# Kernel optimization log

Measured on AMD Instinct MI355X. Metric: run time of the kernel, lower is better.

Reference implementation:

```python
import jax, jax.numpy as jnp
import numpy as np

NUM_HEADS = 12

def setup_inputs() -> dict:
    key = jax.random.key(0)
    ks = jax.random.split(key, 7)
    B, N, C = 8, 1024, 768
    hd = C // NUM_HEADS
    s = 0.02
    x = jax.random.normal(ks[0], (B, N, C), jnp.float32)
    w_qkv = jax.random.normal(ks[1], (3 * C, C), jnp.float32) * s
    w_v1 = jax.random.normal(ks[2], (C, C), jnp.float32) * s
    w_v2 = jax.random.normal(ks[3], (C, C), jnp.float32) * s
    w_proj = jax.random.normal(ks[4], (C, C), jnp.float32) * s
    b_proj = jnp.zeros((C,), jnp.float32)
    # init: real part ones, imag part zeros, plus small noise so the gate is non-trivial
    base = jnp.concatenate([jnp.ones((1, 1, 1, hd // 2 + 1, 1), jnp.float32),
                            jnp.zeros((1, 1, 1, hd // 2 + 1, 1), jnp.float32)], axis=4)
    complex_weight = base + jax.random.normal(ks[5], base.shape, jnp.float32) * s
    return {"x": x, "w_qkv": w_qkv, "w_v1": w_v1, "w_v2": w_v2,
            "w_proj": w_proj, "b_proj": b_proj, "complex_weight": complex_weight}


def reference(x, w_qkv, w_v1, w_v2, w_proj, b_proj, complex_weight):
    B, N, C = x.shape
    H = NUM_HEADS
    hd = C // H
    scale = hd ** -0.5

    qkv = (x @ w_qkv.T).reshape(B, N, 3, H, hd).transpose(2, 0, 3, 1, 4)
    q, k, v = qkv[0], qkv[1], qkv[2]  # [B,H,N,hd]

    # standard softmax attention (dropout p=0 -> identity)
    attn = jax.nn.softmax(jnp.einsum('bhid,bhjd->bhij', q, k) * scale, axis=-1)

    # graph-Laplacian branch: full-channel Q K^T, symmetrized, ReLU'd
    attn_hat = jnp.einsum('bhid,bhjd->bij', q, k)  # [B,N,N]
    attn_hat = jax.nn.relu((attn_hat + attn_hat.transpose(0, 2, 1)) * 0.5)

    # degree normalization: d -> 1/sqrt(d) where d != 0
    deg = attn_hat.sum(axis=2)  # [B,N]
    dinv = jnp.where(deg != 0, jax.lax.rsqrt(jnp.where(deg != 0, deg, 1.0)), 0.0)
    norm_ah = attn_hat * dinv[:, None, :] * dinv[:, :, None]

    I = jnp.eye(N, dtype=x.dtype)[None]  # [1,N,N]
    L = I - norm_ah
    L2 = jnp.matmul(L - I, L - I)  # == norm_ah @ norm_ah

    v_flat = v.transpose(0, 2, 1, 3).reshape(B, N, C)
    out = jnp.matmul(L2 - I, v_flat) @ w_v1.T - jnp.matmul(L2, v_flat) @ w_v2.T

    # FFT spectral gate on V along head_dim
    weight = complex_weight[..., 0] + 1j * complex_weight[..., 1]  # [1,1,1,hd//2+1]
    fft_v = jnp.fft.rfft(v, axis=3, norm='ortho') * weight
    ifft_v = jnp.fft.irfft(fft_v, n=hd, axis=3, norm='ortho')

    y = jnp.einsum('bhij,bhjd->bhid', attn, ifft_v).transpose(0, 2, 1, 3).reshape(B, N, C)
    y = y @ w_proj.T + b_proj
    return (y + out, attn)
```

## Files before the change

### kernel.cpp

```cpp
#include <hip/hip_runtime.h>
#include <math.h>

#define Bb 8
#define Nn 1024
#define Cc 768
#define Hh 12
#define HD 64
#define LD 2304

typedef __attribute__((ext_vector_type(4))) float f32x4;
typedef __attribute__((ext_vector_type(8))) short bf16x8;
typedef unsigned short u16;

__device__ __forceinline__ u16 f2bf(float x) {
    unsigned u = __float_as_uint(x);
    return (u16)((u + 0x7FFFu + ((u >> 16) & 1u)) >> 16);
}
__device__ __forceinline__ float bf2f(u16 h) {
    return __uint_as_float(((unsigned)h) << 16);
}
__device__ __forceinline__ void split4(float4 v, ushort4& h, ushort4& l) {
    h.x = f2bf(v.x); l.x = f2bf(v.x - bf2f(h.x));
    h.y = f2bf(v.y); l.y = f2bf(v.y - bf2f(h.y));
    h.z = f2bf(v.z); l.z = f2bf(v.z - bf2f(h.z));
    h.w = f2bf(v.w); l.w = f2bf(v.w - bf2f(h.w));
}

template<int BM, int BN, int WGM, int WGN, int CA, int OUT>
__global__ __launch_bounds__(WGM * WGN * 64)
void gemm_ms(const u16* __restrict__ Ah, const u16* __restrict__ Al,
             const float* __restrict__ Af, int lda, long sA1, long sA2,
             const u16* __restrict__ Bh, const u16* __restrict__ Bl,
             int ldb, long sB1, long sB2,
             float* __restrict__ C, u16* __restrict__ Ch, u16* __restrict__ Cl,
             int ldc, long sC1, long sC2,
             const float* __restrict__ add, const float* __restrict__ bias,
             int K, int zdiv, float alpha, int accum)
{
    constexpr int T  = WGM * WGN * 64;
    constexpr int BK = 32;
    constexpr int LK = 40;
    constexpr int WM = BM / WGM, WN = BN / WGN;
    constexpr int FM = WM / 16, FN = WN / 16;

    __shared__ short Ahs[BM * LK];
    __shared__ short Als[BM * LK];
    __shared__ short Bhs[BN * LK];
    __shared__ short Bls[BN * LK];

    int z = blockIdx.z;
    int b1 = z / zdiv, b2 = z - b1 * zdiv;
    long aoff = (long)b1 * sA1 + (long)b2 * sA2;
    if (CA) { Af += aoff; } else { Ah += aoff; Al += aoff; }
    long boff = (long)b1 * sB1 + (long)b2 * sB2;
    Bh += boff; Bl += boff;
    long coff = (long)b1 * sC1 + (long)b2 * sC2;
    if (OUT != 1) { C += coff; if (add) add += coff; }
    if (OUT >= 1) { Ch += coff; Cl += coff; }

    int m0 = blockIdx.x * BM;
    int n0 = blockIdx.y * BN;
    int tid = threadIdx.x;
    int lane = tid & 63, wid = tid >> 6;
    int wrow = (wid / WGN) * WM;
    int wcol = (wid - (wid / WGN) * WGN) * WN;
    int lr = lane & 15;
    int lk = lane >> 4;

    f32x4 acc[FM][FN] = {};

    for (int k0 = 0; k0 < K; k0 += BK) {
#pragma unroll
        for (int idx = tid; idx < BM * 4; idx += T) {
            int row = idx >> 2, kq = idx & 3;
            if (CA) {
                const float* src = &Af[(long)(m0 + row) * lda + k0 + kq * 8];
                float4 v0 = *(const float4*)src;
                float4 v1 = *(const float4*)(src + 4);
                ushort4 h0, l0, h1, l1; split4(v0, h0, l0); split4(v1, h1, l1);
                *(ushort4*)&Ahs[row * LK + kq * 8]     = h0;
                *(ushort4*)&Ahs[row * LK + kq * 8 + 4] = h1;
                *(ushort4*)&Als[row * LK + kq * 8]     = l0;
                *(ushort4*)&Als[row * LK + kq * 8 + 4] = l1;
            } else {
                long g = (long)(m0 + row) * lda + k0 + kq * 8;
                *(bf16x8*)&Ahs[row * LK + kq * 8] = *(const bf16x8*)&Ah[g];
                *(bf16x8*)&Als[row * LK + kq * 8] = *(const bf16x8*)&Al[g];
            }
        }
#pragma unroll
        for (int idx = tid; idx < BN * 4; idx += T) {
            int row = idx >> 2, kq = idx & 3;
            long g = (long)(n0 + row) * ldb + k0 + kq * 8;
            *(bf16x8*)&Bhs[row * LK + kq * 8] = *(const bf16x8*)&Bh[g];
            *(bf16x8*)&Bls[row * LK + kq * 8] = *(const bf16x8*)&Bl[g];
        }
        __syncthreads();

        bf16x8 ah[FM], al[FM];
#pragma unroll
        for (int fm = 0; fm < FM; ++fm) {
            int off = (wrow + fm * 16 + lr) * LK + lk * 8;
            ah[fm] = *(const bf16x8*)&Ahs[off];
            al[fm] = *(const bf16x8*)&Als[off];
        }
#pragma unroll
        for (int fn = 0; fn < FN; ++fn) {
            int off = (wcol + fn * 16 + lr) * LK + lk * 8;
            bf16x8 bh = *(const bf16x8*)&Bhs[off];
            bf16x8 bl = *(const bf16x8*)&Bls[off];
#pragma unroll
            for (int fm = 0; fm < FM; ++fm) {
                acc[fm][fn] = __builtin_amdgcn_mfma_f32_16x16x32_bf16(ah[fm], bh, acc[fm][fn], 0, 0, 0);
                acc[fm][fn] = __builtin_amdgcn_mfma_f32_16x16x32_bf16(al[fm], bh, acc[fm][fn], 0, 0, 0);
                acc[fm][fn] = __builtin_amdgcn_mfma_f32_16x16x32_bf16(ah[fm], bl, acc[fm][fn], 0, 0, 0);
            }
        }
        __syncthreads();
    }

#pragma unroll
    for (int fm = 0; fm < FM; ++fm) {
#pragma unroll
        for (int fn = 0; fn < FN; ++fn) {
            int col = n0 + wcol + fn * 16 + lr;
            float bv = 0.0f;
            if (OUT != 1) { if (bias) bv = bias[col]; }
#pragma unroll
            for (int r = 0; r < 4; ++r) {
                int row = m0 + wrow + fm * 16 + lk * 4 + r;
                long idx = (long)row * ldc + col;
                float v = alpha * acc[fm][fn][r];
                if (OUT != 1) {
                    if (accum) v += C[idx];
                    v += bv;
                    if (add) v += add[idx];
                    C[idx] = v;
                }
                if (OUT >= 1) {
                    u16 hh = f2bf(v);
                    Ch[idx] = hh;
                    Cl[idx] = f2bf(v - bf2f(hh));
                }
            }
        }
    }
}

__device__ inline float waveReduceSum(float v) {
#pragma unroll
    for (int off = 32; off; off >>= 1) v += __shfl_down(v, off, 64);
    return v;
}
__device__ inline float waveReduceMax(float v) {
#pragma unroll
    for (int off = 32; off; off >>= 1) v = fmaxf(v, __shfl_down(v, off, 64));
    return v;
}

__global__ __launch_bounds__(256)
void softmax_rows(float* __restrict__ p)
{
    long row = blockIdx.x;
    float* r = p + row * 1024;
    int tid = threadIdx.x;
    float4 x = ((float4*)r)[tid];
    float m = fmaxf(fmaxf(x.x, x.y), fmaxf(x.z, x.w));
    m = waveReduceMax(m);
    __shared__ float sm[4];
    __shared__ float bm, bs;
    int lane = tid & 63, wid = tid >> 6;
    if (!lane) sm[wid] = m;
    __syncthreads();
    if (tid == 0) bm = fmaxf(fmaxf(sm[0], sm[1]), fmaxf(sm[2], sm[3]));
    __syncthreads();
    float mm = bm;
    x.x = expf(x.x - mm); x.y = expf(x.y - mm);
    x.z = expf(x.z - mm); x.w = expf(x.w - mm);
    float s = x.x + x.y + x.z + x.w;
    s = waveReduceSum(s);
    if (!lane) sm[wid] = s;
    __syncthreads();
    if (tid == 0) bs = sm[0] + sm[1] + sm[2] + sm[3];
    __syncthreads();
    float inv = 1.0f / bs;
    x.x *= inv; x.y *= inv; x.z *= inv; x.w *= inv;
    ((float4*)r)[tid] = x;
}

__global__ __launch_bounds__(256)
void sym_relu(float* __restrict__ AH)
{
    long idx = (long)blockIdx.x * 256 + threadIdx.x;
    if (idx >= (long)Bb * Nn * Nn) return;
    int b = (int)(idx >> 20);
    int r = (int)(idx & 1048575);
    int i = r >> 10, j = r & 1023;
    if (j < i) return;
    float* Ab = AH + ((long)b << 20);
    float t = 0.5f * (Ab[i * 1024 + j] + Ab[j * 1024 + i]);
    t = fmaxf(t, 0.0f);
    Ab[i * 1024 + j] = t;
    Ab[j * 1024 + i] = t;
}

__global__ __launch_bounds__(256)
void deg_dinv(const float* __restrict__ AH, float* __restrict__ dinv)
{
    long row = blockIdx.x;
    const float* r = AH + row * 1024;
    int tid = threadIdx.x;
    float4 x = ((const float4*)r)[tid];
    float s = x.x + x.y + x.z + x.w;
    s = waveReduceSum(s);
    __shared__ float sm[4];
    int lane = tid & 63, wid = tid >> 6;
    if (!lane) sm[wid] = s;
    __syncthreads();
    if (tid == 0) {
        float d = sm[0] + sm[1] + sm[2] + sm[3];
        dinv[row] = (d != 0.0f) ? rsqrtf(d) : 0.0f;
    }
}

__global__ __launch_bounds__(256)
void scale_split(const float* __restrict__ AH, const float* __restrict__ dinv,
                 u16* __restrict__ oh, u16* __restrict__ ol)
{
    long i4 = (long)blockIdx.x * 256 + threadIdx.x;
    if (i4 >= (long)Bb * Nn * Nn / 4) return;
    long e = i4 * 4;
    int b = (int)(e >> 20);
    int i = (int)((e >> 10) & 1023);
    int j = (int)(e & 1023);
    float di = dinv[(b << 10) + i];
    const float* dj = &dinv[(b << 10) + j];
    float4 v = ((const float4*)AH)[i4];
    v.x *= di * dj[0]; v.y *= di * dj[1]; v.z *= di * dj[2]; v.w *= di * dj[3];
    ushort4 h, l; split4(v, h, l);
    ((ushort4*)oh)[i4] = h;
    ((ushort4*)ol)[i4] = l;
}

__global__ __launch_bounds__(256)
void split_plain(const float* __restrict__ in, u16* __restrict__ h,
                 u16* __restrict__ l, long n4)
{
    for (long i = (long)blockIdx.x * 256 + threadIdx.x; i < n4;
         i += (long)gridDim.x * 256) {
        float4 v = ((const float4*)in)[i];
        ushort4 hh, ll; split4(v, hh, ll);
        ((ushort4*)h)[i] = hh;
        ((ushort4*)l)[i] = ll;
    }
}

__global__ __launch_bounds__(256)
void wdiff_split(const float* __restrict__ a, const float* __restrict__ b,
                 u16* __restrict__ h, u16* __restrict__ l, long n4)
{
    for (long i = (long)blockIdx.x * 256 + threadIdx.x; i < n4;
         i += (long)gridDim.x * 256) {
        float4 va = ((const float4*)a)[i];
        float4 vb = ((const float4*)b)[i];
        float4 v = make_float4(va.x - vb.x, va.y - vb.y, va.z - vb.z, va.w - vb.w);
        ushort4 hh, ll; split4(v, hh, ll);
        ((ushort4*)h)[i] = hh;
        ((ushort4*)l)[i] = ll;
    }
}

__global__ __launch_bounds__(256)
void tsplit(const float* __restrict__ in, long sIn, int ldi,
            u16* __restrict__ oh, u16* __restrict__ ol, long sOut, int R)
{
    __shared__ float Ts[64][65];
    int z = blockIdx.z;
    in += (long)z * sIn;
    oh += (long)z * sOut;
    ol += (long)z * sOut;
    int r0 = blockIdx.x * 64;
    int c0 = blockIdx.y * 64;
    int tid = threadIdx.x;
#pragma unroll
    for (int idx = tid; idx < 1024; idx += 256) {
        int r = idx >> 4, c4 = idx & 15;
        float4 v = *(const float4*)&in[(long)(r0 + r) * ldi + c0 + c4 * 4];
        Ts[c4 * 4 + 0][r] = v.x;
        Ts[c4 * 4 + 1][r] = v.y;
        Ts[c4 * 4 + 2][r] = v.z;
        Ts[c4 * 4 + 3][r] = v.w;
    }
    __syncthreads();
#pragma unroll
    for (int idx = tid; idx < 1024; idx += 256) {
        int c = idx >> 4, r4 = idx & 15;
        float4 v = make_float4(Ts[c][r4 * 4], Ts[c][r4 * 4 + 1],
                               Ts[c][r4 * 4 + 2], Ts[c][r4 * 4 + 3]);
        ushort4 h, l; split4(v, h, l);
        long o = (long)(c0 + c) * R + r0 + r4 * 4;
        *(ushort4*)&oh[o] = h;
        *(ushort4*)&ol[o] = l;
    }
}

__global__ void build_g(const float* __restrict__ cw, float* __restrict__ g)
{
    int d = threadIdx.x;
    if (d >= 64) return;
    float s = cw[0] + ((d & 1) ? -cw[64] : cw[64]);
#pragma unroll
    for (int f = 1; f < 32; ++f) {
        int ph = (f * d) & 63;
        float ang = 6.283185307179586f * (float)ph / 64.0f;
        s += 2.0f * (cw[2 * f] * cosf(ang) + cw[2 * f + 1] * sinf(ang));
    }
    g[d] = s * 0.015625f;
}

__global__ __launch_bounds__(256)
void ifv_kernel(const float* __restrict__ qkv, const float* __restrict__ g,
                float* __restrict__ ifv)
{
    int bn = blockIdx.x;
    __shared__ float Vr[768];
    __shared__ float Gs[64];
    const float* vrow = qkv + (long)bn * LD + 2 * Cc;
    int tid = threadIdx.x;
    if (tid < 64) Gs[tid] = g[tid];
    for (int c = tid; c < 768; c += 256) Vr[c] = vrow[c];
    __syncthreads();
    for (int c = tid; c < 768; c += 256) {
        int h = c >> 6, t = c & 63;
        const float* vh = Vr + (h << 6);
        float s = 0.0f;
#pragma unroll
        for (int m2 = 0; m2 < 64; ++m2)
            s = fmaf(vh[m2], Gs[(m2 - t) & 63], s);
        ifv[(long)bn * 768 + c] = s;
    }
}

extern "C" void kernel_launch(void* const* d_in, const int* in_sizes, int n_in,
                              void* d_out, int out_size, void* d_ws, size_t ws_size,
                              hipStream_t stream)
{
    (void)in_sizes; (void)n_in; (void)out_size; (void)ws_size;

    const float* x      = (const float*)d_in[0];
    const float* w_qkv  = (const float*)d_in[1];
    const float* w_v1   = (const float*)d_in[2];
    const float* w_v2   = (const float*)d_in[3];
    const float* w_proj = (const float*)d_in[4];
    const float* b_proj = (const float*)d_in[5];
    const float* cw     = (const float*)d_in[6];

    float* out  = (float*)d_out;
    float* attn = out + (long)Bb * Nn * Cc;

    char* W = (char*)d_ws;
    long off = 0;
    auto alloc = [&](long bytes) { char* p = W + off; off += (bytes + 255) & ~255L; return p; };

    float* QKVf  = (float*)alloc((long)8192 * 2304 * 4);
    u16*   QKVh  = (u16*)  alloc((long)8192 * 2304 * 2);
    u16*   QKVl  = (u16*)  alloc((long)8192 * 2304 * 2);
    u16*   AHh   = (u16*)  alloc((long)Bb * Nn * Nn * 2);
    u16*   AHl   = (u16*)  alloc((long)Bb * Nn * Nn * 2);
    u16*   L2h   = (u16*)  alloc((long)Bb * Nn * Nn * 2);
    u16*   L2l   = (u16*)  alloc((long)Bb * Nn * Nn * 2);
    u16*   MVh   = (u16*)  alloc((long)8192 * 768 * 2);
    u16*   MVl   = (u16*)  alloc((long)8192 * 768 * 2);
    float* IFVf  = (float*)alloc((long)8192 * 768 * 4);
    u16*   IFVTh = (u16*)  alloc((long)Bb * 768 * 1024 * 2);
    u16*   IFVTl = (u16*)  alloc((long)Bb * 768 * 1024 * 2);
    u16*   VTh   = (u16*)  alloc((long)Bb * 768 * 1024 * 2);
    u16*   VTl   = (u16*)  alloc((long)Bb * 768 * 1024 * 2);
    u16*   Yh    = (u16*)  alloc((long)8192 * 768 * 2);
    u16*   Yl    = (u16*)  alloc((long)8192 * 768 * 2);
    float* OUTB  = (float*)alloc((long)8192 * 768 * 4);
    u16*   xh    = (u16*)  alloc((long)8192 * 768 * 2);
    u16*   xl    = (u16*)  alloc((long)8192 * 768 * 2);
    u16*   wqh   = (u16*)  alloc((long)2304 * 768 * 2);
    u16*   wql   = (u16*)  alloc((long)2304 * 768 * 2);
    u16*   wv1h  = (u16*)  alloc((long)768 * 768 * 2);
    u16*   wv1l  = (u16*)  alloc((long)768 * 768 * 2);
    u16*   wdh   = (u16*)  alloc((long)768 * 768 * 2);
    u16*   wdl   = (u16*)  alloc((long)768 * 768 * 2);
    u16*   wph   = (u16*)  alloc((long)768 * 768 * 2);
    u16*   wpl   = (u16*)  alloc((long)768 * 768 * 2);
    float* DINV  = (float*)alloc(8192 * 4);
    float* G     = (float*)alloc(256);

    float* AH = attn;

    const long sQKV = (long)Nn * LD;
    const long sNN  = (long)Nn * Nn;
    const long sNC  = (long)Nn * Cc;

    build_g<<<1, 64, 0, stream>>>(cw, G);
    split_plain<<<2048, 256, 0, stream>>>(x,      xh,   xl,   (long)8192 * 768 / 4);
    split_plain<<<1024, 256, 0, stream>>>(w_qkv,  wqh,  wql,  (long)2304 * 768 / 4);
    split_plain<<<512,  256, 0, stream>>>(w_v1,   wv1h, wv1l, (long)768 * 768 / 4);
    split_plain<<<512,  256, 0, stream>>>(w_proj, wph,  wpl,  (long)768 * 768 / 4);
    wdiff_split<<<512,  256, 0, stream>>>(w_v1, w_v2, wdh, wdl, (long)768 * 768 / 4);

    gemm_ms<128, 128, 2, 2, 0, 2><<<dim3(64, 18, 1), 256, 0, stream>>>(
        xh, xl, nullptr, Cc, 0, 0, wqh, wql, Cc, 0, 0,
        QKVf, QKVh, QKVl, LD, 0, 0, nullptr, nullptr, Cc, 1, 1.0f, 0);

    gemm_ms<128, 128, 2, 2, 0, 0><<<dim3(8, 8, Bb), 256, 0, stream>>>(
        QKVh, QKVl, nullptr, LD, sQKV, 0, QKVh + Cc, QKVl + Cc, LD, sQKV, 0,
        AH, nullptr, nullptr, Nn, sNN, 0, nullptr, nullptr, Cc, 1, 1.0f, 0);

    sym_relu<<<32768, 256, 0, stream>>>(AH);
    deg_dinv<<<Bb * Nn, 256, 0, stream>>>(AH, DINV);
    scale_split<<<8192, 256, 0, stream>>>(AH, DINV, AHh, AHl);

    gemm_ms<128, 128, 2, 2, 0, 1><<<dim3(8, 8, Bb), 256, 0, stream>>>(
        AHh, AHl, nullptr, Nn, sNN, 0, AHh, AHl, Nn, sNN, 0,
        nullptr, L2h, L2l, Nn, sNN, 0, nullptr, nullptr, Nn, 1, 1.0f, 0);

    tsplit<<<dim3(16, 12, Bb), 256, 0, stream>>>(
        QKVf + 2 * Cc, sQKV, LD, VTh, VTl, (long)Cc * Nn, Nn);
    gemm_ms<128, 128, 2, 2, 0, 1><<<dim3(8, 6, Bb), 256, 0, stream>>>(
        L2h, L2l, nullptr, Nn, sNN, 0, VTh, VTl, Nn, (long)Cc * Nn, 0,
        nullptr, MVh, MVl, Cc, sNC, 0, nullptr, nullptr, Nn, 1, 1.0f, 0);

    ifv_kernel<<<Bb * Nn, 256, 0, stream>>>(QKVf, G, IFVf);
    tsplit<<<dim3(16, 12, Bb), 256, 0, stream>>>(
        IFVf, sNC, Cc, IFVTh, IFVTl, (long)Cc * Nn, Nn);

    gemm_ms<128, 128, 2, 2, 0, 0><<<dim3(64, 6, 1), 256, 0, stream>>>(
        QKVh + 2 * Cc, QKVl + 2 * Cc, nullptr, LD, 0, 0, wv1h, wv1l, Cc, 0, 0,
        OUTB, nullptr, nullptr, Cc, 0, 0, nullptr, nullptr, Cc, 1, -1.0f, 0);
    gemm_ms<128, 128, 2, 2, 0, 0><<<dim3(64, 6, 1), 256, 0, stream>>>(
        MVh, MVl, nullptr, Cc, 0, 0, wdh, wdl, Cc, 0, 0,
        OUTB, nullptr, nullptr, Cc, 0, 0, nullptr, nullptr, Cc, 1, 1.0f, 1);

    gemm_ms<128, 128, 2, 2, 0, 0><<<dim3(8, 8, Bb * Hh), 256, 0, stream>>>(
        QKVh, QKVl, nullptr, LD, sQKV, HD, QKVh + Cc, QKVl + Cc, LD, sQKV, HD,
        attn, nullptr, nullptr, Nn, (long)Hh * sNN, sNN,
        nullptr, nullptr, HD, Hh, 0.125f, 0);

    softmax_rows<<<Bb * Hh * Nn, 256, 0, stream>>>(attn);

    gemm_ms<128, 64, 2, 1, 1, 1><<<dim3(8, 1, Bb * Hh), 128, 0, stream>>>(
        nullptr, nullptr, attn, Nn, (long)Hh * sNN, sNN,
        IFVTh, IFVTl, Nn, (long)Cc * Nn, (long)HD * Nn,
        nullptr, Yh, Yl, Cc, sNC, HD, nullptr, nullptr, Nn, Hh, 1.0f, 0);

    gemm_ms<128, 128, 2, 2, 0, 0><<<dim3(64, 6, 1), 256, 0, stream>>>(
        Yh, Yl, nullptr, Cc, 0, 0, wph, wpl, Cc, 0, 0,
        out, nullptr, nullptr, Cc, 0, 0, OUTB, b_proj, Cc, 1, 1.0f, 0);
}
```

Before: 1.561 ms.

## Reassociate L2·V as A(A·V), GEMM-ize FFT gate, register-prefetch GEMM tiles

Instead of forming the N×N matrix norm_ah² and multiplying it by V, the code computes (V^T·A)^T and then A·(A·V), which removes one N³ GEMM per batch in favour of two N²·C GEMMs. The spectral FFT gate becomes a block-circulant 768×768 matrix applied as a GEMM, and transposition now works on the bf16 hi/lo pairs, so the fp32 QKV buffer and the separate ifv kernel are no longer needed. The GEMM kernel gains a BK template parameter and register-staged global prefetch of the next K tile, with one barrier pair per iteration. Several launches also move to 64×64 tiles with BK=64, which raises block count at the cost of less reuse per tile.

```diff
diff --git a/kernel.cpp b/kernel.cpp
--- a/kernel.cpp
+++ b/kernel.cpp
@@ -26,7 +26,7 @@
     h.w = f2bf(v.w); l.w = f2bf(v.w - bf2f(h.w));
 }
 
-template<int BM, int BN, int WGM, int WGN, int CA, int OUT>
+template<int BM, int BN, int BK, int WGM, int WGN, int CA, int OUT>
 __global__ __launch_bounds__(WGM * WGN * 64)
 void gemm_ms(const u16* __restrict__ Ah, const u16* __restrict__ Al,
              const float* __restrict__ Af, int lda, long sA1, long sA2,
@@ -38,15 +38,15 @@
              int K, int zdiv, float alpha, int accum)
 {
     constexpr int T  = WGM * WGN * 64;
-    constexpr int BK = 32;
-    constexpr int LK = 40;
+    constexpr int LK = BK + 8;
     constexpr int WM = BM / WGM, WN = BN / WGN;
     constexpr int FM = WM / 16, FN = WN / 16;
-
-    __shared__ short Ahs[BM * LK];
-    __shared__ short Als[BM * LK];
-    __shared__ short Bhs[BN * LK];
-    __shared__ short Bls[BN * LK];
+    constexpr int KQ = BK / 8;
+    constexpr int AI = BM * BK / 8 / T;
+    constexpr int BI = BN * BK / 8 / T;
+    constexpr int KS = BK / 32;
+
+    __shared__ short Ahs[BM * LK], Als[BM * LK], Bhs[BN * LK], Bls[BN * LK];
 
     int z = blockIdx.z;
     int b1 = z / zdiv, b2 = z - b1 * zdiv;
@@ -55,8 +55,8 @@
     long boff = (long)b1 * sB1 + (long)b2 * sB2;
     Bh += boff; Bl += boff;
     long coff = (long)b1 * sC1 + (long)b2 * sC2;
-    if (OUT != 1) { C += coff; if (add) add += coff; }
-    if (OUT >= 1) { Ch += coff; Cl += coff; }
+    if (OUT == 0) { C += coff; if (add) add += coff; }
+    else          { Ch += coff; Cl += coff; }
 
     int m0 = blockIdx.x * BM;
     int n0 = blockIdx.y * BN;
@@ -69,54 +69,89 @@
 
     f32x4 acc[FM][FN] = {};
 
-    for (int k0 = 0; k0 < K; k0 += BK) {
-#pragma unroll
-        for (int idx = tid; idx < BM * 4; idx += T) {
-            int row = idx >> 2, kq = idx & 3;
+    bf16x8 rah[AI], ral[AI], rbh[BI], rbl[BI];
+    float4 rfa[AI][2];
+
+    auto LOAD = [&](int k0) {
+#pragma unroll
+        for (int i = 0; i < AI; ++i) {
+            int idx = i * T + tid;
+            int row = idx / KQ, kq = idx - row * KQ;
             if (CA) {
-                const float* src = &Af[(long)(m0 + row) * lda + k0 + kq * 8];
-                float4 v0 = *(const float4*)src;
-                float4 v1 = *(const float4*)(src + 4);
-                ushort4 h0, l0, h1, l1; split4(v0, h0, l0); split4(v1, h1, l1);
+                const float* s = &Af[(long)(m0 + row) * lda + k0 + kq * 8];
+                rfa[i][0] = *(const float4*)s;
+                rfa[i][1] = *(const float4*)(s + 4);
+            } else {
+                long g = (long)(m0 + row) * lda + k0 + kq * 8;
+                rah[i] = *(const bf16x8*)&Ah[g];
+                ral[i] = *(const bf16x8*)&Al[g];
+            }
+        }
+#pragma unroll
+        for (int i = 0; i < BI; ++i) {
+            int idx = i * T + tid;
+            int row = idx / KQ, kq = idx - row * KQ;
+            long g = (long)(n0 + row) * ldb + k0 + kq * 8;
+            rbh[i] = *(const bf16x8*)&Bh[g];
+            rbl[i] = *(const bf16x8*)&Bl[g];
+        }
+    };
+    auto STORE = [&]() {
+#pragma unroll
+        for (int i = 0; i < AI; ++i) {
+            int idx = i * T + tid;
+            int row = idx / KQ, kq = idx - row * KQ;
+            if (CA) {
+                ushort4 h0, l0, h1, l1;
+                split4(rfa[i][0], h0, l0); split4(rfa[i][1], h1, l1);
                 *(ushort4*)&Ahs[row * LK + kq * 8]     = h0;
                 *(ushort4*)&Ahs[row * LK + kq * 8 + 4] = h1;
                 *(ushort4*)&Als[row * LK + kq * 8]     = l0;
                 *(ushort4*)&Als[row * LK + kq * 8 + 4] = l1;
             } else {
-                long g = (long)(m0 + row) * lda + k0 + kq * 8;
-                *(bf16x8*)&Ahs[row * LK + kq * 8] = *(const bf16x8*)&Ah[g];
-                *(bf16x8*)&Als[row * LK + kq * 8] = *(const bf16x8*)&Al[g];
+                *(bf16x8*)&Ahs[row * LK + kq * 8] = rah[i];
+                *(bf16x8*)&Als[row * LK + kq * 8] = ral[i];
             }
         }
 #pragma unroll
-        for (int idx = tid; idx < BN * 4; idx += T) {
-            int row = idx >> 2, kq = idx & 3;
-            long g = (long)(n0 + row) * ldb + k0 + kq * 8;
-            *(bf16x8*)&Bhs[row * LK + kq * 8] = *(const bf16x8*)&Bh[g];
-            *(bf16x8*)&Bls[row * LK + kq * 8] = *(const bf16x8*)&Bl[g];
-        }
+        for (int i = 0; i < BI; ++i) {
+            int idx = i * T + tid;
+            int row = idx / KQ, kq = idx - row * KQ;
+            *(bf16x8*)&Bhs[row * LK + kq * 8] = rbh[i];
+            *(bf16x8*)&Bls[row * LK + kq * 8] = rbl[i];
+        }
+    };
+
+    int nt = K / BK;
+    LOAD(0);
+    for (int t = 0; t < nt; ++t) {
         __syncthreads();
-
-        bf16x8 ah[FM], al[FM];
-#pragma unroll
-        for (int fm = 0; fm < FM; ++fm) {
-            int off = (wrow + fm * 16 + lr) * LK + lk * 8;
-            ah[fm] = *(const bf16x8*)&Ahs[off];
-            al[fm] = *(const bf16x8*)&Als[off];
-        }
-#pragma unroll
-        for (int fn = 0; fn < FN; ++fn) {
-            int off = (wcol + fn * 16 + lr) * LK + lk * 8;
-            bf16x8 bh = *(const bf16x8*)&Bhs[off];
-            bf16x8 bl = *(const bf16x8*)&Bls[off];
+        STORE();
+        __syncthreads();
+        if (t + 1 < nt) LOAD((t + 1) * BK);
+
+#pragma unroll
+        for (int s = 0; s < KS; ++s) {
+            bf16x8 fah[FM], fal[FM];
 #pragma unroll
             for (int fm = 0; fm < FM; ++fm) {
-                acc[fm][fn] = __builtin_amdgcn_mfma_f32_16x16x32_bf16(ah[fm], bh, acc[fm][fn], 0, 0, 0);
-                acc[fm][fn] = __builtin_amdgcn_mfma_f32_16x16x32_bf16(al[fm], bh, acc[fm][fn], 0, 0, 0);
-                acc[fm][fn] = __builtin_amdgcn_mfma_f32_16x16x32_bf16(ah[fm], bl, acc[fm][fn], 0, 0, 0);
+                int off = (wrow + fm * 16 + lr) * LK + s * 32 + lk * 8;
+                fah[fm] = *(const bf16x8*)&Ahs[off];
+                fal[fm] = *(const bf16x8*)&Als[off];
             }
-        }
-        __syncthreads();
+#pragma unroll
+            for (int fn = 0; fn < FN; ++fn) {
+                int off = (wcol + fn * 16 + lr) * LK + s * 32 + lk * 8;
+                bf16x8 fbh = *(const bf16x8*)&Bhs[off];
+                bf16x8 fbl = *(const bf16x8*)&Bls[off];
+#pragma unroll
+                for (int fm = 0; fm < FM; ++fm) {
+                    acc[fm][fn] = __builtin_amdgcn_mfma_f32_16x16x32_bf16(fah[fm], fbh, acc[fm][fn], 0, 0, 0);
+                    acc[fm][fn] = __builtin_amdgcn_mfma_f32_16x16x32_bf16(fal[fm], fbh, acc[fm][fn], 0, 0, 0);
+                    acc[fm][fn] = __builtin_amdgcn_mfma_f32_16x16x32_bf16(fah[fm], fbl, acc[fm][fn], 0, 0, 0);
+                }
+            }
+        }
     }
 
 #pragma unroll
@@ -125,19 +160,18 @@
         for (int fn = 0; fn < FN; ++fn) {
             int col = n0 + wcol + fn * 16 + lr;
             float bv = 0.0f;
-            if (OUT != 1) { if (bias) bv = bias[col]; }
+            if (OUT == 0) { if (bias) bv = bias[col]; }
 #pragma unroll
             for (int r = 0; r < 4; ++r) {
                 int row = m0 + wrow + fm * 16 + lk * 4 + r;
                 long idx = (long)row * ldc + col;
                 float v = alpha * acc[fm][fn][r];
-                if (OUT != 1) {
+                if (OUT == 0) {
                     if (accum) v += C[idx];
                     v += bv;
                     if (add) v += add[idx];
                     C[idx] = v;
-                }
-                if (OUT >= 1) {
+                } else {
                     u16 hh = f2bf(v);
                     Ch[idx] = hh;
                     Cl[idx] = f2bf(v - bf2f(hh));
@@ -271,36 +305,38 @@
 }
 
 __global__ __launch_bounds__(256)
-void tsplit(const float* __restrict__ in, long sIn, int ldi,
-            u16* __restrict__ oh, u16* __restrict__ ol, long sOut, int R)
-{
-    __shared__ float Ts[64][65];
+void t16(const u16* __restrict__ inh, const u16* __restrict__ inl, long sIn, int ldi,
+         u16* __restrict__ oh, u16* __restrict__ ol, long sOut, int R)
+{
+    __shared__ u16 Th[64][68];
+    __shared__ u16 Tl[64][68];
     int z = blockIdx.z;
-    in += (long)z * sIn;
-    oh += (long)z * sOut;
-    ol += (long)z * sOut;
+    inh += (long)z * sIn; inl += (long)z * sIn;
+    oh  += (long)z * sOut; ol += (long)z * sOut;
     int r0 = blockIdx.x * 64;
     int c0 = blockIdx.y * 64;
     int tid = threadIdx.x;
 #pragma unroll
-    for (int idx = tid; idx < 1024; idx += 256) {
-        int r = idx >> 4, c4 = idx & 15;
-        float4 v = *(const float4*)&in[(long)(r0 + r) * ldi + c0 + c4 * 4];
-        Ts[c4 * 4 + 0][r] = v.x;
-        Ts[c4 * 4 + 1][r] = v.y;
-        Ts[c4 * 4 + 2][r] = v.z;
-        Ts[c4 * 4 + 3][r] = v.w;
-    }
-    __syncthreads();
-#pragma unroll
-    for (int idx = tid; idx < 1024; idx += 256) {
-        int c = idx >> 4, r4 = idx & 15;
-        float4 v = make_float4(Ts[c][r4 * 4], Ts[c][r4 * 4 + 1],
-                               Ts[c][r4 * 4 + 2], Ts[c][r4 * 4 + 3]);
-        ushort4 h, l; split4(v, h, l);
-        long o = (long)(c0 + c) * R + r0 + r4 * 4;
-        *(ushort4*)&oh[o] = h;
-        *(ushort4*)&ol[o] = l;
+    for (int i = tid; i < 1024; i += 256) {
+        int r = i >> 4, cq = i & 15;
+        ushort4 vh = *(const ushort4*)&inh[(long)(r0 + r) * ldi + c0 + cq * 4];
+        ushort4 vl = *(const ushort4*)&inl[(long)(r0 + r) * ldi + c0 + cq * 4];
+        Th[cq * 4 + 0][r] = vh.x; Th[cq * 4 + 1][r] = vh.y;
+        Th[cq * 4 + 2][r] = vh.z; Th[cq * 4 + 3][r] = vh.w;
+        Tl[cq * 4 + 0][r] = vl.x; Tl[cq * 4 + 1][r] = vl.y;
+        Tl[cq * 4 + 2][r] = vl.z; Tl[cq * 4 + 3][r] = vl.w;
+    }
+    __syncthreads();
+#pragma unroll
+    for (int i = tid; i < 1024; i += 256) {
+        int c = i >> 4, rq = i & 15;
+        ushort4 vh = make_ushort4(Th[c][rq * 4], Th[c][rq * 4 + 1],
+                                  Th[c][rq * 4 + 2], Th[c][rq * 4 + 3]);
+        ushort4 vl = make_ushort4(Tl[c][rq * 4], Tl[c][rq * 4 + 1],
+                                  Tl[c][rq * 4 + 2], Tl[c][rq * 4 + 3]);
+        long o = (long)(c0 + c) * R + r0 + rq * 4;
+        *(ushort4*)&oh[o] = vh;
+        *(ushort4*)&ol[o] = vl;
     }
 }
 
@@ -319,26 +355,16 @@
 }
 
 __global__ __launch_bounds__(256)
-void ifv_kernel(const float* __restrict__ qkv, const float* __restrict__ g,
-                float* __restrict__ ifv)
-{
-    int bn = blockIdx.x;
-    __shared__ float Vr[768];
-    __shared__ float Gs[64];
-    const float* vrow = qkv + (long)bn * LD + 2 * Cc;
-    int tid = threadIdx.x;
-    if (tid < 64) Gs[tid] = g[tid];
-    for (int c = tid; c < 768; c += 256) Vr[c] = vrow[c];
-    __syncthreads();
-    for (int c = tid; c < 768; c += 256) {
-        int h = c >> 6, t = c & 63;
-        const float* vh = Vr + (h << 6);
-        float s = 0.0f;
-#pragma unroll
-        for (int m2 = 0; m2 < 64; ++m2)
-            s = fmaf(vh[m2], Gs[(m2 - t) & 63], s);
-        ifv[(long)bn * 768 + c] = s;
-    }
+void build_gb(const float* __restrict__ g, u16* __restrict__ gbh, u16* __restrict__ gbl)
+{
+    int idx = blockIdx.x * 256 + threadIdx.x;
+    if (idx >= Cc * Cc) return;
+    int c = idx / Cc, c2 = idx - (idx / Cc) * Cc;
+    int h = c >> 6, t = c & 63, h2 = c2 >> 6, m = c2 & 63;
+    float v = (h == h2) ? g[(m - t) & 63] : 0.0f;
+    u16 hh = f2bf(v);
+    gbh[idx] = hh;
+    gbl[idx] = f2bf(v - bf2f(hh));
 }
 
 extern "C" void kernel_launch(void* const* d_in, const int* in_sizes, int n_in,
@@ -362,20 +388,18 @@
     long off = 0;
     auto alloc = [&](long bytes) { char* p = W + off; off += (bytes + 255) & ~255L; return p; };
 
-    float* QKVf  = (float*)alloc((long)8192 * 2304 * 4);
     u16*   QKVh  = (u16*)  alloc((long)8192 * 2304 * 2);
     u16*   QKVl  = (u16*)  alloc((long)8192 * 2304 * 2);
     u16*   AHh   = (u16*)  alloc((long)Bb * Nn * Nn * 2);
     u16*   AHl   = (u16*)  alloc((long)Bb * Nn * Nn * 2);
-    u16*   L2h   = (u16*)  alloc((long)Bb * Nn * Nn * 2);
-    u16*   L2l   = (u16*)  alloc((long)Bb * Nn * Nn * 2);
+    u16*   VTh   = (u16*)  alloc((long)Bb * Cc * Nn * 2);
+    u16*   VTl   = (u16*)  alloc((long)Bb * Cc * Nn * 2);
+    u16*   W1Th  = (u16*)  alloc((long)Bb * Cc * Nn * 2);
+    u16*   W1Tl  = (u16*)  alloc((long)Bb * Cc * Nn * 2);
     u16*   MVh   = (u16*)  alloc((long)8192 * 768 * 2);
     u16*   MVl   = (u16*)  alloc((long)8192 * 768 * 2);
-    float* IFVf  = (float*)alloc((long)8192 * 768 * 4);
-    u16*   IFVTh = (u16*)  alloc((long)Bb * 768 * 1024 * 2);
-    u16*   IFVTl = (u16*)  alloc((long)Bb * 768 * 1024 * 2);
-    u16*   VTh   = (u16*)  alloc((long)Bb * 768 * 1024 * 2);
-    u16*   VTl   = (u16*)  alloc((long)Bb * 768 * 1024 * 2);
+    u16*   IFVTh = (u16*)  alloc((long)Bb * Cc * Nn * 2);
+    u16*   IFVTl = (u16*)  alloc((long)Bb * Cc * Nn * 2);
     u16*   Yh    = (u16*)  alloc((long)8192 * 768 * 2);
     u16*   Yl    = (u16*)  alloc((long)8192 * 768 * 2);
     float* OUTB  = (float*)alloc((long)8192 * 768 * 4);
@@ -389,6 +413,8 @@
     u16*   wdl   = (u16*)  alloc((long)768 * 768 * 2);
     u16*   wph   = (u16*)  alloc((long)768 * 768 * 2);
     u16*   wpl   = (u16*)  alloc((long)768 * 768 * 2);
+    u16*   gbh   = (u16*)  alloc((long)768 * 768 * 2);
+    u16*   gbl   = (u16*)  alloc((long)768 * 768 * 2);
     float* DINV  = (float*)alloc(8192 * 4);
     float* G     = (float*)alloc(256);
 
@@ -397,19 +423,21 @@
     const long sQKV = (long)Nn * LD;
     const long sNN  = (long)Nn * Nn;
     const long sNC  = (long)Nn * Cc;
+    const long sCN  = (long)Cc * Nn;
 
     build_g<<<1, 64, 0, stream>>>(cw, G);
+    build_gb<<<(Cc * Cc + 255) / 256, 256, 0, stream>>>(G, gbh, gbl);
     split_plain<<<2048, 256, 0, stream>>>(x,      xh,   xl,   (long)8192 * 768 / 4);
     split_plain<<<1024, 256, 0, stream>>>(w_qkv,  wqh,  wql,  (long)2304 * 768 / 4);
     split_plain<<<512,  256, 0, stream>>>(w_v1,   wv1h, wv1l, (long)768 * 768 / 4);
     split_plain<<<512,  256, 0, stream>>>(w_proj, wph,  wpl,  (long)768 * 768 / 4);
     wdiff_split<<<512,  256, 0, stream>>>(w_v1, w_v2, wdh, wdl, (long)768 * 768 / 4);
 
-    gemm_ms<128, 128, 2, 2, 0, 2><<<dim3(64, 18, 1), 256, 0, stream>>>(
+    gemm_ms<128, 128, 32, 2, 2, 0, 1><<<dim3(64, 18, 1), 256, 0, stream>>>(
         xh, xl, nullptr, Cc, 0, 0, wqh, wql, Cc, 0, 0,
-        QKVf, QKVh, QKVl, LD, 0, 0, nullptr, nullptr, Cc, 1, 1.0f, 0);
-
-    gemm_ms<128, 128, 2, 2, 0, 0><<<dim3(8, 8, Bb), 256, 0, stream>>>(
+        nullptr, QKVh, QKVl, LD, 0, 0, nullptr, nullptr, Cc, 1, 1.0f, 0);
+
+    gemm_ms<64, 64, 64, 2, 2, 0, 0><<<dim3(16, 16, Bb), 256, 0, stream>>>(
         QKVh, QKVl, nullptr, LD, sQKV, 0, QKVh + Cc, QKVl + Cc, LD, sQKV, 0,
         AH, nullptr, nullptr, Nn, sNN, 0, nullptr, nullptr, Cc, 1, 1.0f, 0);
 
@@ -417,40 +445,40 @@
     deg_dinv<<<Bb * Nn, 256, 0, stream>>>(AH, DINV);
     scale_split<<<8192, 256, 0, stream>>>(AH, DINV, AHh, AHl);
 
-    gemm_ms<128, 128, 2, 2, 0, 1><<<dim3(8, 8, Bb), 256, 0, stream>>>(
-        AHh, AHl, nullptr, Nn, sNN, 0, AHh, AHl, Nn, sNN, 0,
-        nullptr, L2h, L2l, Nn, sNN, 0, nullptr, nullptr, Nn, 1, 1.0f, 0);
-
-    tsplit<<<dim3(16, 12, Bb), 256, 0, stream>>>(
-        QKVf + 2 * Cc, sQKV, LD, VTh, VTl, (long)Cc * Nn, Nn);
-    gemm_ms<128, 128, 2, 2, 0, 1><<<dim3(8, 6, Bb), 256, 0, stream>>>(
-        L2h, L2l, nullptr, Nn, sNN, 0, VTh, VTl, Nn, (long)Cc * Nn, 0,
+    gemm_ms<64, 64, 64, 2, 2, 0, 1><<<dim3(12, 16, Bb), 256, 0, stream>>>(
+        gbh, gbl, nullptr, Cc, 0, 0, QKVh + 2 * Cc, QKVl + 2 * Cc, LD, sQKV, 0,
+        nullptr, IFVTh, IFVTl, Nn, sCN, 0, nullptr, nullptr, Cc, 1, 1.0f, 0);
+
+    t16<<<dim3(16, 12, Bb), 256, 0, stream>>>(
+        QKVh + 2 * Cc, QKVl + 2 * Cc, sQKV, LD, VTh, VTl, sCN, Nn);
+
+    gemm_ms<64, 64, 64, 2, 2, 0, 1><<<dim3(12, 16, Bb), 256, 0, stream>>>(
+        VTh, VTl, nullptr, Nn, sCN, 0, AHh, AHl, Nn, sNN, 0,
+        nullptr, W1Th, W1Tl, Nn, sCN, 0, nullptr, nullptr, Nn, 1, 1.0f, 0);
+    gemm_ms<64, 64, 64, 2, 2, 0, 1><<<dim3(16, 12, Bb), 256, 0, stream>>>(
+        AHh, AHl, nullptr, Nn, sNN, 0, W1Th, W1Tl, Nn, sCN, 0,
         nullptr, MVh, MVl, Cc, sNC, 0, nullptr, nullptr, Nn, 1, 1.0f, 0);
 
-    ifv_kernel<<<Bb * Nn, 256, 0, stream>>>(QKVf, G, IFVf);
-    tsplit<<<dim3(16, 12, Bb), 256, 0, stream>>>(
-        IFVf, sNC, Cc, IFVTh, IFVTl, (long)Cc * Nn, Nn);
-
-    gemm_ms<128, 128, 2, 2, 0, 0><<<dim3(64, 6, 1), 256, 0, stream>>>(
+    gemm_ms<64, 64, 64, 2, 2, 0, 0><<<dim3(128, 12, 1), 256, 0, stream>>>(
         QKVh + 2 * Cc, QKVl + 2 * Cc, nullptr, LD, 0, 0, wv1h, wv1l, Cc, 0, 0,
         OUTB, nullptr, nullptr, Cc, 0, 0, nullptr, nullptr, Cc, 1, -1.0f, 0);
-    gemm_ms<128, 128, 2, 2, 0, 0><<<dim3(64, 6, 1), 256, 0, stream>>>(
+    gemm_ms<64, 64, 64, 2, 2, 0, 0><<<dim3(128, 12, 1), 256, 0, stream>>>(
         MVh, MVl, nullptr, Cc, 0, 0, wdh, wdl, Cc, 0, 0,
         OUTB, nullptr, nullptr, Cc, 0, 0, nullptr, nullptr, Cc, 1, 1.0f, 1);
 
-    gemm_ms<128, 128, 2, 2, 0, 0><<<dim3(8, 8, Bb * Hh), 256, 0, stream>>>(
+    gemm_ms<128, 128, 32, 2, 2, 0, 0><<<dim3(8, 8, Bb * Hh), 256, 0, stream>>>(
         QKVh, QKVl, nullptr, LD, sQKV, HD, QKVh + Cc, QKVl + Cc, LD, sQKV, HD,
         attn, nullptr, nullptr, Nn, (long)Hh * sNN, sNN,
         nullptr, nullptr, HD, Hh, 0.125f, 0);
 
     softmax_rows<<<Bb * Hh * Nn, 256, 0, stream>>>(attn);
 
-    gemm_ms<128, 64, 2, 1, 1, 1><<<dim3(8, 1, Bb * Hh), 128, 0, stream>>>(
+    gemm_ms<64, 64, 64, 2, 2, 1, 1><<<dim3(16, 1, Bb * Hh), 256, 0, stream>>>(
         nullptr, nullptr, attn, Nn, (long)Hh * sNN, sNN,
-        IFVTh, IFVTl, Nn, (long)Cc * Nn, (long)HD * Nn,
+        IFVTh, IFVTl, Nn, sCN, (long)HD * Nn,
         nullptr, Yh, Yl, Cc, sNC, HD, nullptr, nullptr, Nn, Hh, 1.0f, 0);
 
-    gemm_ms<128, 128, 2, 2, 0, 0><<<dim3(64, 6, 1), 256, 0, stream>>>(
+    gemm_ms<64, 64, 64, 2, 2, 0, 0><<<dim3(128, 12, 1), 256, 0, stream>>>(
         Yh, Yl, nullptr, Cc, 0, 0, wph, wpl, Cc, 0, 0,
         out, nullptr, nullptr, Cc, 0, 0, OUTB, b_proj, Cc, 1, 1.0f, 0);
 }
```

Measured after the change: 1.350 ms. 1.16x faster.
